# Optimization experiments

Measured on AMD Instinct MI355X. Metric: run time of the kernel, lower is better.

## Reference

```python
import jax, jax.numpy as jnp
import numpy as np

NEG_INF = jnp.float32(-9e15)

def gat_layer(x, adj_mask, W, a, alpha):
    # x: [N, F_in]; W: [H, F_in, F_out]; a: [H, 2*F_out]; adj_mask: [N, N] bool
    H, _, O = W.shape
    h = jnp.einsum('nf,hfo->hno', x, W)            # [H, N, O]
    a_src, a_dst = a[:, :O], a[:, O:]              # [H, O] each
    e_src = jnp.einsum('hno,ho->hn', h, a_src)     # [H, N]
    e_dst = jnp.einsum('hno,ho->hn', h, a_dst)     # [H, N]
    e = jax.nn.leaky_relu(e_src[:, :, None] + e_dst[:, None, :], negative_slope=alpha)
    e = jnp.where(adj_mask[None, :, :], e, NEG_INF)  # mask non-edges
    attn = jax.nn.softmax(e, axis=-1)              # [H, N, N]
    out = jnp.einsum('hnm,hmo->hno', attn, h)      # [H, N, O]
    return out.mean(axis=0)                        # average heads -> [N, O]

def setup_inputs() -> dict:
    key = jax.random.key(0)
    ks = jax.random.split(key, 6)
    N, F_IN, F_HID, F_CLS, H = 4096, 512, 256, 16, 4
    x = jax.random.normal(ks[0], (N, F_IN), dtype=jnp.float32)
    adj = jax.random.randint(ks[1], (N, N), 0, 2, dtype=jnp.int32)
    W1 = jax.random.normal(ks[2], (H, F_IN, F_HID), dtype=jnp.float32) * 0.05
    a1 = jax.random.normal(ks[3], (H, 2 * F_HID), dtype=jnp.float32) * 0.05
    W2 = jax.random.normal(ks[4], (1, F_HID, F_CLS), dtype=jnp.float32) * 0.05
    a2 = jax.random.normal(ks[5], (1, 2 * F_CLS), dtype=jnp.float32) * 0.05
    return {"x": x, "adj": adj, "W1": W1, "a1": a1, "W2": W2, "a2": a2}

def reference(x, adj, W1, a1, W2, a2):
    alpha = 0.2
    adj_mask = adj > 0
    h = jax.nn.relu(gat_layer(x, adj_mask, W1, a1, alpha))        # layer1 + ReLU
    out = gat_layer(h, adj_mask, W2, a2, alpha)                    # layer2
    return jax.nn.log_softmax(out, axis=1)                         # [N, nclass]
```

## Files before the change

### kernel.cpp

```cpp
#include <hip/hip_runtime.h>
#include <stdint.h>

#define N_NODES 4096
#define F_IN    512
#define F_HID   256
#define F_CLS   16
#define NHEAD   4
#define ALPHA   0.2f
#define LOG2E   1.4426950408889634f

typedef __attribute__((ext_vector_type(8))) short short8;
typedef __attribute__((ext_vector_type(4))) float f32x4;

__device__ __forceinline__ float bf2f(unsigned short h) {
    unsigned u = ((unsigned)h) << 16; float f; __builtin_memcpy(&f, &u, 4); return f;
}
__device__ __forceinline__ unsigned short f2bf(float f) {
    unsigned u; __builtin_memcpy(&u, &f, 4);
    u += 0x7fffu + ((u >> 16) & 1u);
    return (unsigned short)(u >> 16);
}
__device__ __forceinline__ float lo_bf(unsigned u) { u <<= 16;          float f; __builtin_memcpy(&f,&u,4); return f; }
__device__ __forceinline__ float hi_bf(unsigned u) { u &= 0xffff0000u;  float f; __builtin_memcpy(&f,&u,4); return f; }

__device__ __forceinline__ void async_cp16(void* lds, const void* g) {
    __builtin_amdgcn_global_load_lds(
        (const __attribute__((address_space(1))) unsigned int*)g,
        (__attribute__((address_space(3))) unsigned int*)lds,
        16, 0, 0);
}

__device__ __forceinline__ void pipe_barrier_vm2() {
    __builtin_amdgcn_sched_barrier(0);
    __builtin_amdgcn_s_waitcnt(0x0072);
    __builtin_amdgcn_s_barrier();
    __builtin_amdgcn_sched_barrier(0);
}
__device__ __forceinline__ void pipe_barrier_vm3() {
    __builtin_amdgcn_sched_barrier(0);
    __builtin_amdgcn_s_waitcnt(0x0073);
    __builtin_amdgcn_s_barrier();
    __builtin_amdgcn_sched_barrier(0);
}

#define PREP_BM_BLOCKS   16384
#define PREP_CV_BLOCKS   1296
#define PREP_Z_BLOCKS    4
__global__ __launch_bounds__(256) void k_prep(const int* __restrict__ adj,
                                              const float* __restrict__ x,
                                              const float* __restrict__ W1,
                                              const float* __restrict__ W2,
                                              unsigned long long* __restrict__ bm,
                                              unsigned short* __restrict__ xb,
                                              unsigned short* __restrict__ W1t,
                                              float* __restrict__ W2t,
                                              float* __restrict__ ez) {
    int b = blockIdx.x;
    if (b < PREP_BM_BLOCKS) {
        int wv = threadIdx.x >> 6, lane = threadIdx.x & 63;
        int idx0 = b * 1024 + wv * 256;
        const int* p = adj + idx0 + lane;
        unsigned long long m0 = __ballot(p[0]   > 0);
        unsigned long long m1 = __ballot(p[64]  > 0);
        unsigned long long m2 = __ballot(p[128] > 0);
        unsigned long long m3 = __ballot(p[192] > 0);
        if (lane == 0) {
            int w = idx0 >> 6;
            bm[w] = m0; bm[w+1] = m1; bm[w+2] = m2; bm[w+3] = m3;
        }
        return;
    }
    if (b < PREP_BM_BLOCKS + PREP_CV_BLOCKS) {
        int tid = (b - PREP_BM_BLOCKS) * 256 + threadIdx.x;
        const int NXV = (N_NODES * F_IN) / 8;
        const int NW1 = NHEAD * 64 * F_HID;
        if (tid < NXV) {
            float4 a = *(const float4*)&x[tid * 8];
            float4 c = *(const float4*)&x[tid * 8 + 4];
            uint4 w;
            w.x = (unsigned)f2bf(a.x) | ((unsigned)f2bf(a.y) << 16);
            w.y = (unsigned)f2bf(a.z) | ((unsigned)f2bf(a.w) << 16);
            w.z = (unsigned)f2bf(c.x) | ((unsigned)f2bf(c.y) << 16);
            w.w = (unsigned)f2bf(c.z) | ((unsigned)f2bf(c.w) << 16);
            *(uint4*)&xb[tid * 8] = w;
        } else if (tid < NXV + NW1) {
            int j = tid - NXV;
            int o = j & 255, f8 = (j >> 8) & 63, h = j >> 14;
            float v[8];
            #pragma unroll
            for (int k = 0; k < 8; ++k)
                v[k] = W1[(size_t)(h * F_IN + f8 * 8 + k) * F_HID + o];
            uint4 w;
            w.x = (unsigned)f2bf(v[0]) | ((unsigned)f2bf(v[1]) << 16);
            w.y = (unsigned)f2bf(v[2]) | ((unsigned)f2bf(v[3]) << 16);
            w.z = (unsigned)f2bf(v[4]) | ((unsigned)f2bf(v[5]) << 16);
            w.w = (unsigned)f2bf(v[6]) | ((unsigned)f2bf(v[7]) << 16);
            *(uint4*)&W1t[(size_t)(h * F_HID + o) * F_IN + f8 * 8] = w;
        } else {
            int j = tid - NXV - NW1;
            if (j < F_HID * F_CLS) {
                int o = j >> 4, c = j & 15;
                W2t[c * F_HID + o] = W2[j];
            }
        }
        return;
    }
    {
        int zb = b - PREP_BM_BLOCKS - PREP_CV_BLOCKS;
        float4* z4 = (float4*)ez;
        #pragma unroll
        for (int r = 0; r < 8; ++r)
            z4[zb * 2048 + r * 256 + threadIdx.x] = make_float4(0.f, 0.f, 0.f, 0.f);
    }
}

__global__ __launch_bounds__(256, 4) void k_gemm1(const unsigned short* __restrict__ xb,
                                                  const unsigned short* __restrict__ W1t,
                                                  const float* __restrict__ a1,
                                                  unsigned short* __restrict__ h1t,
                                                  float* __restrict__ es1,
                                                  float* __restrict__ ed1) {
    __shared__ unsigned short Sld[3][6144];
    const int t = threadIdx.x;
    const int lane = t & 63, wv = t >> 6, quad = lane >> 4, l15 = lane & 15;
    const int wn = wv & 1, wo = wv >> 1;
    const int n0 = blockIdx.x * 128;
    const int oo0 = blockIdx.y * 64;
    const int h = blockIdx.z;
    const int kl = (lane >> 4) * 8;

    const unsigned short* gs[3];
    int loff[3];
    #pragma unroll
    for (int s = 0; s < 3; ++s) {
        int c = wv * 3 + s;
        loff[s] = c * 512;
        gs[s] = (c < 8)
            ? (xb  + (size_t)(n0 + c * 16 + l15) * F_IN + kl)
            : (W1t + (size_t)(h * F_HID + oo0 + (c - 8) * 16 + l15) * F_IN + kl);
    }
    #pragma unroll
    for (int s = 0; s < 3; ++s) async_cp16(&Sld[0][loff[s]], gs[s]);
    #pragma unroll
    for (int s = 0; s < 3; ++s) async_cp16(&Sld[1][loff[s]], gs[s] + 32);

    f32x4 acc[4][2] = {};
    int cur = 0;
    for (int it = 0; it < 16; ++it) {
        pipe_barrier_vm3();
        {
            const int nxt = (cur >= 1) ? cur - 1 : 2;
            const int off = ((it + 2) & 15) * 32;
            #pragma unroll
            for (int s = 0; s < 3; ++s) async_cp16(&Sld[nxt][loff[s]], gs[s] + off);
        }
        short8 bfw[2];
        #pragma unroll
        for (int mi = 0; mi < 2; ++mi)
            bfw[mi] = *(const short8*)&Sld[cur][(8 + wo * 2 + mi) * 512 + lane * 8];
        #pragma unroll
        for (int ni = 0; ni < 4; ++ni) {
            short8 af = *(const short8*)&Sld[cur][(wn * 4 + ni) * 512 + lane * 8];
            #pragma unroll
            for (int mi = 0; mi < 2; ++mi)
                acc[ni][mi] = __builtin_amdgcn_mfma_f32_16x16x32_bf16(af, bfw[mi], acc[ni][mi], 0, 0, 0);
        }
        cur = (cur == 2) ? 0 : cur + 1;
    }
    #pragma unroll
    for (int ni = 0; ni < 4; ++ni)
      #pragma unroll
      for (int mi = 0; mi < 2; ++mi) {
        int o = oo0 + wo * 32 + mi * 16 + l15;
        int nb = n0 + wn * 64 + ni * 16 + quad * 4;
        uint2 uu;
        uu.x = (unsigned)f2bf(acc[ni][mi][0]) | ((unsigned)f2bf(acc[ni][mi][1]) << 16);
        uu.y = (unsigned)f2bf(acc[ni][mi][2]) | ((unsigned)f2bf(acc[ni][mi][3]) << 16);
        *(uint2*)&h1t[(size_t)(h * F_HID + o) * N_NODES + nb] = uu;
      }
    float a1s[2], a1d[2];
    #pragma unroll
    for (int mi = 0; mi < 2; ++mi) {
        int o = oo0 + wo * 32 + mi * 16 + l15;
        a1s[mi] = a1[h * 2 * F_HID + o] * LOG2E;
        a1d[mi] = a1[h * 2 * F_HID + F_HID + o] * LOG2E;
    }
    #pragma unroll
    for (int ni = 0; ni < 4; ++ni) {
        #pragma unroll
        for (int rg = 0; rg < 4; ++rg) {
            float es = acc[ni][0][rg] * a1s[0] + acc[ni][1][rg] * a1s[1];
            float ed = acc[ni][0][rg] * a1d[0] + acc[ni][1][rg] * a1d[1];
            #pragma unroll
            for (int off = 1; off < 16; off <<= 1) {
                es += __shfl_xor(es, off, 64);
                ed += __shfl_xor(ed, off, 64);
            }
            if (l15 == 0) {
                int n = n0 + wn * 64 + ni * 16 + quad * 4 + rg;
                atomicAdd(&es1[h * N_NODES + n], es);
                atomicAdd(&ed1[h * N_NODES + n], ed);
            }
        }
    }
}

__global__ __launch_bounds__(512, 2) void k_attn1(const unsigned short* __restrict__ h1t,
                                                  const float* __restrict__ es1,
                                                  const float* __restrict__ ed1,
                                                  const unsigned char* __restrict__ bmb,
                                                  unsigned short* __restrict__ C1p,
                                                  float* __restrict__ l1p) {
    __shared__ unsigned short Bld[3][8192];
    const int t = threadIdx.x;
    const int lane = t & 63, wv = t >> 6, quad = lane >> 4, l15 = lane & 15;
    const int m0 = blockIdx.x * 256;
    const int h = blockIdx.y;
    const int kz = blockIdx.z;
    const int mb0 = kz * 1024;

    const int m_r0 = m0 + wv * 32 + l15;
    const int m_r1 = m_r0 + 16;
    const float esr0 = es1[h * N_NODES + m_r0];
    const float esr1 = es1[h * N_NODES + m_r1];
    const unsigned char* bp0 = bmb + (size_t)m_r0 * (N_NODES / 8) + (mb0 >> 3);
    const unsigned char* bp1 = bmb + (size_t)m_r1 * (N_NODES / 8) + (mb0 >> 3);
    const float* edb = ed1 + h * N_NODES + mb0;

    const unsigned short* gb0 = h1t + (size_t)(h * F_HID + wv * 16 + l15) * N_NODES + mb0 + quad * 8;
    const unsigned short* gb1 = h1t + (size_t)(h * F_HID + (wv + 8) * 16 + l15) * N_NODES + mb0 + quad * 8;
    async_cp16(&Bld[0][wv * 512], gb0);
    async_cp16(&Bld[0][(wv + 8) * 512], gb1);
    async_cp16(&Bld[1][wv * 512], gb0 + 32);
    async_cp16(&Bld[1][(wv + 8) * 512], gb1 + 32);

    f32x4 acc[16][2] = {};
    float lsum0 = 0.f, lsum1 = 0.f;
    int cur = 0;
    for (int it = 0; it < 32; ++it) {
        const int mb = it * 32;
        pipe_barrier_vm2();
        float4 e0 = *(const float4*)&edb[mb + quad * 8];
        float4 e1v = *(const float4*)&edb[mb + quad * 8 + 4];
        unsigned bb0 = bp0[(mb >> 3) + quad];
        unsigned bb1 = bp1[(mb >> 3) + quad];
        __builtin_amdgcn_sched_barrier(0);
        {
            const int nxt = (cur >= 1) ? cur - 1 : 2;
            const int mbp = ((it + 2) & 31) * 32;
            async_cp16(&Bld[nxt][wv * 512], gb0 + mbp);
            async_cp16(&Bld[nxt][(wv + 8) * 512], gb1 + mbp);
        }
        __builtin_amdgcn_sched_barrier(0);
        float ev[8] = {e0.x, e0.y, e0.z, e0.w, e1v.x, e1v.y, e1v.z, e1v.w};
        unsigned up0[8], up1[8];
        #pragma unroll
        for (int j = 0; j < 8; ++j) {
            float s0 = esr0 + ev[j]; s0 = fmaxf(s0, ALPHA * s0);
            float p0 = ((bb0 >> j) & 1u) ? __builtin_amdgcn_exp2f(s0) : 0.f;
            unsigned u0; __builtin_memcpy(&u0, &p0, 4); u0 &= 0xffff0000u;
            float pt0; __builtin_memcpy(&pt0, &u0, 4);
            lsum0 += pt0; up0[j] = u0;
            float s1 = esr1 + ev[j]; s1 = fmaxf(s1, ALPHA * s1);
            float p1 = ((bb1 >> j) & 1u) ? __builtin_amdgcn_exp2f(s1) : 0.f;
            unsigned u1; __builtin_memcpy(&u1, &p1, 4); u1 &= 0xffff0000u;
            float pt1; __builtin_memcpy(&pt1, &u1, 4);
            lsum1 += pt1; up1[j] = u1;
        }
        int pk0[4], pk1[4];
        #pragma unroll
        for (int j = 0; j < 4; ++j) {
            pk0[j] = __builtin_amdgcn_perm(up0[2*j+1], up0[2*j], 0x07060302u);
            pk1[j] = __builtin_amdgcn_perm(up1[2*j+1], up1[2*j], 0x07060302u);
        }
        short8 bfrag0, bfrag1;
        __builtin_memcpy(&bfrag0, pk0, 16);
        __builtin_memcpy(&bfrag1, pk1, 16);
        #pragma unroll
        for (int ot = 0; ot < 16; ++ot) {
            short8 af = *(const short8*)&Bld[cur][ot * 512 + lane * 8];
            acc[ot][0] = __builtin_amdgcn_mfma_f32_16x16x32_bf16(af, bfrag0, acc[ot][0], 0, 0, 0);
            acc[ot][1] = __builtin_amdgcn_mfma_f32_16x16x32_bf16(af, bfrag1, acc[ot][1], 0, 0, 0);
        }
        cur = (cur == 2) ? 0 : cur + 1;
    }
    lsum0 += __shfl_xor(lsum0, 16, 64); lsum0 += __shfl_xor(lsum0, 32, 64);
    lsum1 += __shfl_xor(lsum1, 16, 64); lsum1 += __shfl_xor(lsum1, 32, 64);
    if (quad == 0) {
        l1p[(size_t)(kz * NHEAD + h) * N_NODES + m_r0] = lsum0;
        l1p[(size_t)(kz * NHEAD + h) * N_NODES + m_r1] = lsum1;
    }
    unsigned short* Cb = C1p + (size_t)(kz * NHEAD + h) * N_NODES * F_HID;
    #pragma unroll
    for (int ot = 0; ot < 16; ++ot)
      #pragma unroll
      for (int mi = 0; mi < 2; ++mi) {
        int m = (mi == 0) ? m_r0 : m_r1;
        int o0 = ot * 16 + quad * 4;
        uint2 uu;
        uu.x = (unsigned)f2bf(acc[ot][mi][0]) | ((unsigned)f2bf(acc[ot][mi][1]) << 16);
        uu.y = (unsigned)f2bf(acc[ot][mi][2]) | ((unsigned)f2bf(acc[ot][mi][3]) << 16);
        *(uint2*)&Cb[(size_t)m * F_HID + o0] = uu;
      }
}

__global__ __launch_bounds__(256) void k_reduce_h2w(const unsigned short* __restrict__ C1p,
                                                    const float* __restrict__ l1p,
                                                    const float* __restrict__ W2t,
                                                    const float* __restrict__ a2,
                                                    unsigned short* __restrict__ h2wt,
                                                    float* __restrict__ es2,
                                                    float* __restrict__ ed2) {
    __shared__ float h2s[8][256];
    int t = threadIdx.x;
    int og = t & 31, nl = t >> 5;
    int n = blockIdx.x * 8 + nl;
    float acc8[8] = {};
    #pragma unroll
    for (int h = 0; h < NHEAD; ++h) {
        float den = 0.f, num[8] = {};
        #pragma unroll
        for (int kz = 0; kz < 4; ++kz) {
            den += l1p[(size_t)(kz * NHEAD + h) * N_NODES + n];
            uint4 u = *(const uint4*)&C1p[((size_t)(kz * NHEAD + h) * N_NODES + n) * F_HID + og * 8];
            num[0] += lo_bf(u.x); num[1] += hi_bf(u.x);
            num[2] += lo_bf(u.y); num[3] += hi_bf(u.y);
            num[4] += lo_bf(u.z); num[5] += hi_bf(u.z);
            num[6] += lo_bf(u.w); num[7] += hi_bf(u.w);
        }
        float rinv = 1.f / fmaxf(den, 1e-30f);
        #pragma unroll
        for (int j = 0; j < 8; ++j) acc8[j] += num[j] * rinv;
    }
    #pragma unroll
    for (int j = 0; j < 8; ++j) {
        float v = fmaxf(acc8[j] * 0.25f, 0.f);
        h2s[nl][og * 8 + j] = bf2f(f2bf(v));
    }
    __syncthreads();
    if (t < 128) {
        int c = t & 15, n2l = t >> 4;
        int n2 = blockIdx.x * 8 + n2l;
        const float* wrow = W2t + c * F_HID;
        const float* hrow = h2s[n2l];
        float dot = 0.f;
        #pragma unroll 4
        for (int o = 0; o < F_HID; o += 8) {
            float4 hv0 = *(const float4*)&hrow[o];
            float4 hv1 = *(const float4*)&hrow[o + 4];
            float4 w0 = *(const float4*)&wrow[o];
            float4 w1 = *(const float4*)&wrow[o + 4];
            dot += hv0.x*w0.x + hv0.y*w0.y + hv0.z*w0.z + hv0.w*w0.w;
            dot += hv1.x*w1.x + hv1.y*w1.y + hv1.z*w1.z + hv1.w*w1.w;
        }
        h2wt[(size_t)c * N_NODES + n2] = f2bf(dot);
        float es = dot * a2[c] * LOG2E;
        float ed = dot * a2[F_CLS + c] * LOG2E;
        #pragma unroll
        for (int off = 1; off < 16; off <<= 1) {
            es += __shfl_xor(es, off, 64);
            ed += __shfl_xor(ed, off, 64);
        }
        if (c == 0) { es2[n2] = es; ed2[n2] = ed; }
    }
}

__global__ __launch_bounds__(256, 4) void k_attn2(const unsigned short* __restrict__ h2wt,
                                                  const float* __restrict__ es2,
                                                  const float* __restrict__ ed2,
                                                  const unsigned char* __restrict__ bmb,
                                                  float* __restrict__ out2p,
                                                  float* __restrict__ l2p) {
    const int t = threadIdx.x;
    const int lane = t & 63, wv = t >> 6, quad = lane >> 4, l15 = lane & 15;
    const int m0 = blockIdx.x * 64;
    const int ks = blockIdx.y;
    const int m_r = m0 + wv * 16 + l15;
    const float esr = es2[m_r];
    const unsigned char* bp = bmb + (size_t)m_r * (N_NODES / 8);

    f32x4 acc = {};
    float lsum = 0.f;
    for (int it = 0; it < 16; ++it) {
        const int mb = ks * 512 + it * 32;
        float4 e0 = *(const float4*)&ed2[mb + quad * 8];
        float4 e1v = *(const float4*)&ed2[mb + quad * 8 + 4];
        float ev[8] = {e0.x, e0.y, e0.z, e0.w, e1v.x, e1v.y, e1v.z, e1v.w};
        unsigned bb = bp[(mb >> 3) + quad];
        short8 afrag;
        #pragma unroll
        for (int j = 0; j < 8; ++j) {
            float s = esr + ev[j]; s = fmaxf(s, ALPHA * s);
            float p = ((bb >> j) & 1u) ? __builtin_amdgcn_exp2f(s) : 0.f;
            lsum += p; afrag[j] = (short)f2bf(p);
        }
        short8 bfr = *(const short8*)&h2wt[(size_t)l15 * N_NODES + mb + quad * 8];
        acc = __builtin_amdgcn_mfma_f32_16x16x32_bf16(afrag, bfr, acc, 0, 0, 0);
    }
    lsum += __shfl_xor(lsum, 16, 64); lsum += __shfl_xor(lsum, 32, 64);
    if (quad == 0) l2p[(size_t)ks * N_NODES + m_r] = lsum;
    #pragma unroll
    for (int rg = 0; rg < 4; ++rg) {
        int row = m0 + wv * 16 + quad * 4 + rg;
        out2p[((size_t)ks * N_NODES + row) * F_CLS + l15] = acc[rg];
    }
}

__global__ __launch_bounds__(256) void k_final(const float* __restrict__ out2p,
                                               const float* __restrict__ l2p,
                                               float* __restrict__ out) {
    int t = threadIdx.x;
    int c = t & 15, nl = t >> 4;
    int n = blockIdx.x * 16 + nl;
    float v = 0.f, l = 0.f;
    #pragma unroll
    for (int ks = 0; ks < 8; ++ks) {
        v += out2p[((size_t)ks * N_NODES + n) * F_CLS + c];
        l += l2p[(size_t)ks * N_NODES + n];
    }
    v /= fmaxf(l, 1e-30f);
    float mx = v;
    #pragma unroll
    for (int off = 1; off < 16; off <<= 1) mx = fmaxf(mx, __shfl_xor(mx, off, 64));
    float e = __expf(v - mx);
    float se = e;
    #pragma unroll
    for (int off = 1; off < 16; off <<= 1) se += __shfl_xor(se, off, 64);
    out[(size_t)n * F_CLS + c] = v - mx - __logf(se);
}

#define OFF_BM    0ull
#define OFF_XB    2097152ull
#define OFF_W1T   6291456ull
#define OFF_W2T   7340032ull
#define OFF_ES1   7356416ull
#define OFF_ED1   7421952ull
#define OFF_ES2   7487488ull
#define OFF_ED2   7503872ull
#define OFF_L1P   7520256ull
#define OFF_L2P   7782400ull
#define OFF_OUT2P 7910400ull
#define OFF_H2WT  10007552ull
#define OFF_H1T   10138624ull
#define OFF_C1P   18527232ull

extern "C" void kernel_launch(void* const* d_in, const int* in_sizes, int n_in,
                              void* d_out, int out_size, void* d_ws, size_t ws_size,
                              hipStream_t stream) {
    const float* x   = (const float*)d_in[0];
    const int*   adj = (const int*)d_in[1];
    const float* W1  = (const float*)d_in[2];
    const float* a1  = (const float*)d_in[3];
    const float* W2  = (const float*)d_in[4];
    const float* a2  = (const float*)d_in[5];
    float* out = (float*)d_out;
    char* ws = (char*)d_ws;

    unsigned long long* bm  = (unsigned long long*)(ws + OFF_BM);
    unsigned char*      bmb = (unsigned char*)(ws + OFF_BM);
    unsigned short* xb   = (unsigned short*)(ws + OFF_XB);
    unsigned short* W1t  = (unsigned short*)(ws + OFF_W1T);
    float* W2t   = (float*)(ws + OFF_W2T);
    float* es1   = (float*)(ws + OFF_ES1);
    float* ed1   = (float*)(ws + OFF_ED1);
    float* es2   = (float*)(ws + OFF_ES2);
    float* ed2   = (float*)(ws + OFF_ED2);
    float* l1p   = (float*)(ws + OFF_L1P);
    float* l2p   = (float*)(ws + OFF_L2P);
    float* out2p = (float*)(ws + OFF_OUT2P);
    unsigned short* h2wt = (unsigned short*)(ws + OFF_H2WT);
    unsigned short* h1t  = (unsigned short*)(ws + OFF_H1T);
    unsigned short* C1p  = (unsigned short*)(ws + OFF_C1P);

    k_prep       <<<dim3(PREP_BM_BLOCKS + PREP_CV_BLOCKS + PREP_Z_BLOCKS), 256, 0, stream>>>(
                     adj, x, W1, W2, bm, xb, W1t, W2t, es1);
    k_gemm1      <<<dim3(32, 4, 4), 256, 0, stream>>>(xb, W1t, a1, h1t, es1, ed1);
    k_attn1      <<<dim3(16, 4, 4), 512, 0, stream>>>(h1t, es1, ed1, bmb, C1p, l1p);
    k_reduce_h2w <<<dim3(512),      256, 0, stream>>>(C1p, l1p, W2t, a2, h2wt, es2, ed2);
    k_attn2      <<<dim3(64, 8),    256, 0, stream>>>(h2wt, es2, ed2, bmb, out2p, l2p);
    k_final      <<<dim3(256),      256, 0, stream>>>(out2p, l2p, out);
}
```

Before: 228.7 us.

## Drop LDS pipeline in attn1; load h1 fragments directly with 4 row-frags per wave

The first-layer attention kernel no longer stages h1t tiles through a triple-buffered LDS async-copy pipeline with block barriers. Each wave now reads its MFMA A-fragments straight from global memory and computes four 16-row P fragments instead of two, so every loaded h1 fragment feeds four MFMAs. The block shrinks to 256 threads with one block per SIMD group, removing barrier synchronisation. The cost is a doubled accumulator register footprint (64 f32x4 per wave), lower occupancy, and global-load latency no longer hidden by explicit prefetch. All 16 waves' worth of h1 traffic is now issued by each of four waves, raising per-wave L2 load pressure.

Result: slower. 319.6 us (+39.7%).

```diff
diff --git a/kernel.cpp b/kernel.cpp
--- a/kernel.cpp
+++ b/kernel.cpp
@@ -30,12 +30,6 @@
         16, 0, 0);
 }
 
-__device__ __forceinline__ void pipe_barrier_vm2() {
-    __builtin_amdgcn_sched_barrier(0);
-    __builtin_amdgcn_s_waitcnt(0x0072);
-    __builtin_amdgcn_s_barrier();
-    __builtin_amdgcn_sched_barrier(0);
-}
 __device__ __forceinline__ void pipe_barrier_vm3() {
     __builtin_amdgcn_sched_barrier(0);
     __builtin_amdgcn_s_waitcnt(0x0073);
@@ -205,13 +199,12 @@
     }
 }
 
-__global__ __launch_bounds__(512, 2) void k_attn1(const unsigned short* __restrict__ h1t,
+__global__ __launch_bounds__(256, 1) void k_attn1(const unsigned short* __restrict__ h1t,
                                                   const float* __restrict__ es1,
                                                   const float* __restrict__ ed1,
                                                   const unsigned char* __restrict__ bmb,
                                                   unsigned short* __restrict__ C1p,
                                                   float* __restrict__ l1p) {
-    __shared__ unsigned short Bld[3][8192];
     const int t = threadIdx.x;
     const int lane = t & 63, wv = t >> 6, quad = lane >> 4, l15 = lane & 15;
     const int m0 = blockIdx.x * 256;
@@ -219,88 +212,69 @@
     const int kz = blockIdx.z;
     const int mb0 = kz * 1024;
 
-    const int m_r0 = m0 + wv * 32 + l15;
-    const int m_r1 = m_r0 + 16;
-    const float esr0 = es1[h * N_NODES + m_r0];
-    const float esr1 = es1[h * N_NODES + m_r1];
-    const unsigned char* bp0 = bmb + (size_t)m_r0 * (N_NODES / 8) + (mb0 >> 3);
-    const unsigned char* bp1 = bmb + (size_t)m_r1 * (N_NODES / 8) + (mb0 >> 3);
+    int m_r[4];
+    float esr[4];
+    const unsigned char* bp[4];
+    #pragma unroll
+    for (int rf = 0; rf < 4; ++rf) {
+        m_r[rf] = m0 + wv * 64 + rf * 16 + l15;
+        esr[rf] = es1[h * N_NODES + m_r[rf]];
+        bp[rf] = bmb + (size_t)m_r[rf] * (N_NODES / 8) + (mb0 >> 3);
+    }
     const float* edb = ed1 + h * N_NODES + mb0;
-
-    const unsigned short* gb0 = h1t + (size_t)(h * F_HID + wv * 16 + l15) * N_NODES + mb0 + quad * 8;
-    const unsigned short* gb1 = h1t + (size_t)(h * F_HID + (wv + 8) * 16 + l15) * N_NODES + mb0 + quad * 8;
-    async_cp16(&Bld[0][wv * 512], gb0);
-    async_cp16(&Bld[0][(wv + 8) * 512], gb1);
-    async_cp16(&Bld[1][wv * 512], gb0 + 32);
-    async_cp16(&Bld[1][(wv + 8) * 512], gb1 + 32);
-
-    f32x4 acc[16][2] = {};
-    float lsum0 = 0.f, lsum1 = 0.f;
-    int cur = 0;
+    const unsigned short* hb = h1t + (size_t)(h * F_HID + l15) * N_NODES + mb0 + quad * 8;
+
+    f32x4 acc[16][4] = {};
+    float lsum[4] = {};
     for (int it = 0; it < 32; ++it) {
         const int mb = it * 32;
-        pipe_barrier_vm2();
         float4 e0 = *(const float4*)&edb[mb + quad * 8];
         float4 e1v = *(const float4*)&edb[mb + quad * 8 + 4];
-        unsigned bb0 = bp0[(mb >> 3) + quad];
-        unsigned bb1 = bp1[(mb >> 3) + quad];
-        __builtin_amdgcn_sched_barrier(0);
-        {
-            const int nxt = (cur >= 1) ? cur - 1 : 2;
-            const int mbp = ((it + 2) & 31) * 32;
-            async_cp16(&Bld[nxt][wv * 512], gb0 + mbp);
-            async_cp16(&Bld[nxt][(wv + 8) * 512], gb1 + mbp);
-        }
-        __builtin_amdgcn_sched_barrier(0);
         float ev[8] = {e0.x, e0.y, e0.z, e0.w, e1v.x, e1v.y, e1v.z, e1v.w};
-        unsigned up0[8], up1[8];
-        #pragma unroll
-        for (int j = 0; j < 8; ++j) {
-            float s0 = esr0 + ev[j]; s0 = fmaxf(s0, ALPHA * s0);
-            float p0 = ((bb0 >> j) & 1u) ? __builtin_amdgcn_exp2f(s0) : 0.f;
-            unsigned u0; __builtin_memcpy(&u0, &p0, 4); u0 &= 0xffff0000u;
-            float pt0; __builtin_memcpy(&pt0, &u0, 4);
-            lsum0 += pt0; up0[j] = u0;
-            float s1 = esr1 + ev[j]; s1 = fmaxf(s1, ALPHA * s1);
-            float p1 = ((bb1 >> j) & 1u) ? __builtin_amdgcn_exp2f(s1) : 0.f;
-            unsigned u1; __builtin_memcpy(&u1, &p1, 4); u1 &= 0xffff0000u;
-            float pt1; __builtin_memcpy(&pt1, &u1, 4);
-            lsum1 += pt1; up1[j] = u1;
-        }
-        int pk0[4], pk1[4];
-        #pragma unroll
-        for (int j = 0; j < 4; ++j) {
-            pk0[j] = __builtin_amdgcn_perm(up0[2*j+1], up0[2*j], 0x07060302u);
-            pk1[j] = __builtin_amdgcn_perm(up1[2*j+1], up1[2*j], 0x07060302u);
-        }
-        short8 bfrag0, bfrag1;
-        __builtin_memcpy(&bfrag0, pk0, 16);
-        __builtin_memcpy(&bfrag1, pk1, 16);
+        short8 bfrag[4];
+        #pragma unroll
+        for (int rf = 0; rf < 4; ++rf) {
+            unsigned bb = bp[rf][(mb >> 3) + quad];
+            unsigned up[8];
+            #pragma unroll
+            for (int j = 0; j < 8; ++j) {
+                float s = esr[rf] + ev[j]; s = fmaxf(s, ALPHA * s);
+                float p = ((bb >> j) & 1u) ? __builtin_amdgcn_exp2f(s) : 0.f;
+                unsigned u; __builtin_memcpy(&u, &p, 4); u &= 0xffff0000u;
+                float pt; __builtin_memcpy(&pt, &u, 4);
+                lsum[rf] += pt; up[j] = u;
+            }
+            int pk[4];
+            #pragma unroll
+            for (int j = 0; j < 4; ++j)
+                pk[j] = __builtin_amdgcn_perm(up[2*j+1], up[2*j], 0x07060302u);
+            __builtin_memcpy(&bfrag[rf], pk, 16);
+        }
         #pragma unroll
         for (int ot = 0; ot < 16; ++ot) {
-            short8 af = *(const short8*)&Bld[cur][ot * 512 + lane * 8];
-            acc[ot][0] = __builtin_amdgcn_mfma_f32_16x16x32_bf16(af, bfrag0, acc[ot][0], 0, 0, 0);
-            acc[ot][1] = __builtin_amdgcn_mfma_f32_16x16x32_bf16(af, bfrag1, acc[ot][1], 0, 0, 0);
-        }
-        cur = (cur == 2) ? 0 : cur + 1;
-    }
-    lsum0 += __shfl_xor(lsum0, 16, 64); lsum0 += __shfl_xor(lsum0, 32, 64);
-    lsum1 += __shfl_xor(lsum1, 16, 64); lsum1 += __shfl_xor(lsum1, 32, 64);
-    if (quad == 0) {
-        l1p[(size_t)(kz * NHEAD + h) * N_NODES + m_r0] = lsum0;
-        l1p[(size_t)(kz * NHEAD + h) * N_NODES + m_r1] = lsum1;
+            short8 af = *(const short8*)&hb[(size_t)ot * 16 * N_NODES + mb];
+            #pragma unroll
+            for (int rf = 0; rf < 4; ++rf)
+                acc[ot][rf] = __builtin_amdgcn_mfma_f32_16x16x32_bf16(af, bfrag[rf], acc[ot][rf], 0, 0, 0);
+        }
+    }
+    #pragma unroll
+    for (int rf = 0; rf < 4; ++rf) {
+        lsum[rf] += __shfl_xor(lsum[rf], 16, 64);
+        lsum[rf] += __shfl_xor(lsum[rf], 32, 64);
+        if (quad == 0)
+            l1p[(size_t)(kz * NHEAD + h) * N_NODES + m_r[rf]] = lsum[rf];
     }
     unsigned short* Cb = C1p + (size_t)(kz * NHEAD + h) * N_NODES * F_HID;
     #pragma unroll
     for (int ot = 0; ot < 16; ++ot)
       #pragma unroll
-      for (int mi = 0; mi < 2; ++mi) {
-        int m = (mi == 0) ? m_r0 : m_r1;
+      for (int rf = 0; rf < 4; ++rf) {
         int o0 = ot * 16 + quad * 4;
         uint2 uu;
-        uu.x = (unsigned)f2bf(acc[ot][mi][0]) | ((unsigned)f2bf(acc[ot][mi][1]) << 16);
-        uu.y = (unsigned)f2bf(acc[ot][mi][2]) | ((unsigned)f2bf(acc[ot][mi][3]) << 16);
-        *(uint2*)&Cb[(size_t)m * F_HID + o0] = uu;
+        uu.x = (unsigned)f2bf(acc[ot][rf][0]) | ((unsigned)f2bf(acc[ot][rf][1]) << 16);
+        uu.y = (unsigned)f2bf(acc[ot][rf][2]) | ((unsigned)f2bf(acc[ot][rf][3]) << 16);
+        *(uint2*)&Cb[(size_t)m_r[rf] * F_HID + o0] = uu;
       }
 }
 
@@ -475,7 +449,7 @@
     k_prep       <<<dim3(PREP_BM_BLOCKS + PREP_CV_BLOCKS + PREP_Z_BLOCKS), 256, 0, stream>>>(
                      adj, x, W1, W2, bm, xb, W1t, W2t, es1);
     k_gemm1      <<<dim3(32, 4, 4), 256, 0, stream>>>(xb, W1t, a1, h1t, es1, ed1);
-    k_attn1      <<<dim3(16, 4, 4), 512, 0, stream>>>(h1t, es1, ed1, bmb, C1p, l1p);
+    k_attn1      <<<dim3(16, 4, 4), 256, 0, stream>>>(h1t, es1, ed1, bmb, C1p, l1p);
     k_reduce_h2w <<<dim3(512),      256, 0, stream>>>(C1p, l1p, W2t, a2, h2wt, es2, ed2);
     k_attn2      <<<dim3(64, 8),    256, 0, stream>>>(h2wt, es2, ed2, bmb, out2p, l2p);
     k_final      <<<dim3(256),      256, 0, stream>>>(out2p, l2p, out);
```
